# Performance work log

Hardware: AMD Instinct MI355X
Metric: run time of the kernel (lower is better)

## Reference

```python
import jax, jax.numpy as jnp
import numpy as np

EPS = 1e-05
IN_FEATURES = 1024
OUT_FEATURES = 512
M = 65536


def setup_inputs() -> dict:
    key = jax.random.key(0)
    k_x, k_w, k_b = jax.random.split(key, 3)
    x = jax.random.normal(k_x, (M, IN_FEATURES), dtype=jnp.float32)
    # kaiming_uniform(a=sqrt(5)) on [out, in]: bound = sqrt(6/((1+a^2)*fan_in)) = 1/sqrt(fan_in)
    bound = 1.0 / np.sqrt(IN_FEATURES)
    weight = jax.random.uniform(k_w, (OUT_FEATURES, IN_FEATURES), dtype=jnp.float32,
                                minval=-bound, maxval=bound)
    bias = jax.random.uniform(k_b, (OUT_FEATURES,), dtype=jnp.float32,
                              minval=-bound, maxval=bound)
    gamma = jnp.ones((OUT_FEATURES,), dtype=jnp.float32)
    beta = jnp.zeros((OUT_FEATURES,), dtype=jnp.float32)
    scale = jnp.ones((1,), dtype=jnp.float32)
    return {"x": x, "weight": weight, "bias": bias,
            "gamma": gamma, "beta": beta, "scale": scale}


def reference(x, weight, bias, gamma, beta, scale):
    # GEMM + bias: [M, N]
    acc = jnp.einsum('mk,nk->mn', x, weight) + bias[None, :]
    # Row-wise normalization over N (as the fused kernel computes per row)
    mean = jnp.mean(acc, axis=1, keepdims=True)
    var = jnp.mean((acc - mean) ** 2, axis=1, keepdims=True)
    normalized = (acc - mean) / jnp.sqrt(var + EPS)
    scaled = (normalized * gamma[None, :] + beta[None, :]) * scale[0]
    # Row softmax over N
    return jax.nn.softmax(scaled, axis=1)
```

## Files before the change

kernel.cpp:

```cpp
#include <hip/hip_runtime.h>
#include <hip/hip_bf16.h>

constexpr int KD = 1024;
constexpr int ND = 512;
constexpr int NT = 32;
constexpr float EPSV = 1e-5f;

using f32x4  = __attribute__((ext_vector_type(4))) float;
using bf16x8 = __attribute__((ext_vector_type(8))) short;
using u16x8  = __attribute__((ext_vector_type(8))) unsigned short;

__device__ __forceinline__ unsigned short f2bf(float f) {
  unsigned int u = __builtin_bit_cast(unsigned int, f);
  return (unsigned short)((u + 0x7fffu + ((u >> 16) & 1u)) >> 16);
}

__device__ __forceinline__ u16x8 pack8(float4 a, float4 b) {
  u16x8 v;
  v[0] = f2bf(a.x); v[1] = f2bf(a.y); v[2] = f2bf(a.z); v[3] = f2bf(a.w);
  v[4] = f2bf(b.x); v[5] = f2bf(b.y); v[6] = f2bf(b.z); v[7] = f2bf(b.w);
  return v;
}

__device__ __forceinline__ unsigned short cvt1(float f) {
  __hip_bfloat16 h = __float2bfloat16(f);
  return __builtin_bit_cast(unsigned short, h);
}

#define SCHEDB()  __builtin_amdgcn_sched_barrier(0)

#define BARRIER() do { \
    asm volatile("s_waitcnt lgkmcnt(0)" ::: "memory"); \
    __builtin_amdgcn_sched_barrier(0); \
    __builtin_amdgcn_s_barrier(); \
    __builtin_amdgcn_sched_barrier(0); } while (0)

__global__ void wconvert_kernel(const float* __restrict__ w,
                                unsigned short* __restrict__ wb) {
  int uid = blockIdx.x * blockDim.x + threadIdx.x;
  int s   = uid >> 11;
  int nf  = (uid >> 6) & 31;
  int l   = uid & 63;
  int n   = nf * 16 + (l & 15);
  int k0  = s * 32 + (l >> 4) * 8;
  const float* src = w + n * KD + k0;
  float4 a = *reinterpret_cast<const float4*>(src);
  float4 b = *reinterpret_cast<const float4*>(src + 4);
  *reinterpret_cast<u16x8*>(wb + (size_t)uid * 8) = pack8(a, b);
}

__global__ __launch_bounds__(512, 4)
void fused_kernel(const float* __restrict__ x,
                  const unsigned short* __restrict__ wb,
                  const float* __restrict__ bias,
                  const float* __restrict__ gamma,
                  const float* __restrict__ beta,
                  const float* __restrict__ scalep,
                  float* __restrict__ out) {
  __shared__ unsigned short As[8][64 * 32];

  const int tid  = threadIdx.x;
  const int lane = tid & 63;
  const int wid  = tid >> 6;
  const int l15  = lane & 15;
  const int lg   = lane >> 4;

  const long bm  = (long)blockIdx.x * 64;

  f32x4 acc[4][4] = {};

  const int arow = tid >> 3;
  const int akq  = tid & 7;
  const float* asrc = x + (bm + arow) * KD + akq * 4;
  const int awb = arow * 64 + (((akq >> 1) ^ ((arow >> 1) & 3)) * 16)
                + ((akq & 1) * 8);

  const int swa = (lg ^ ((l15 >> 1) & 3)) * 16;
  int ard[4];
  #pragma unroll
  for (int mi = 0; mi < 4; ++mi) ard[mi] = (mi * 16 + l15) * 64 + swa;

  const unsigned short* bbase = wb + ((size_t)(wid * 4) * 64 + lane) * 8;

#define LOADA(t) (*reinterpret_cast<const float4*>(asrc + (t) * 32))

#define LOADB(t, r0, r1, r2, r3) do { \
    const unsigned short* bp_ = bbase + (size_t)(t) * 16384; \
    r0 = *reinterpret_cast<const bf16x8*>(bp_ + 0 * 512); \
    r1 = *reinterpret_cast<const bf16x8*>(bp_ + 1 * 512); \
    r2 = *reinterpret_cast<const bf16x8*>(bp_ + 2 * 512); \
    r3 = *reinterpret_cast<const bf16x8*>(bp_ + 3 * 512); } while (0)

#define WRITE_A(q_, bufi) do { \
    union { unsigned short s[4]; unsigned long long v; } c_; \
    c_.s[0] = cvt1(q_.x); c_.s[1] = cvt1(q_.y); \
    c_.s[2] = cvt1(q_.z); c_.s[3] = cvt1(q_.w); \
    *reinterpret_cast<unsigned long long*>((char*)As[bufi] + awb) = c_.v; } while (0)

#define COMPUTE(bufi, B0, B1, B2, B3) do { \
    const char* ab_ = (const char*)As[bufi]; \
    bf16x8 a0_ = *reinterpret_cast<const bf16x8*>(ab_ + ard[0]); \
    bf16x8 a1_ = *reinterpret_cast<const bf16x8*>(ab_ + ard[1]); \
    bf16x8 a2_ = *reinterpret_cast<const bf16x8*>(ab_ + ard[2]); \
    bf16x8 a3_ = *reinterpret_cast<const bf16x8*>(ab_ + ard[3]); \
    acc[0][0] = __builtin_amdgcn_mfma_f32_16x16x32_bf16(a0_, B0, acc[0][0], 0, 0, 0); \
    acc[0][1] = __builtin_amdgcn_mfma_f32_16x16x32_bf16(a0_, B1, acc[0][1], 0, 0, 0); \
    acc[0][2] = __builtin_amdgcn_mfma_f32_16x16x32_bf16(a0_, B2, acc[0][2], 0, 0, 0); \
    acc[0][3] = __builtin_amdgcn_mfma_f32_16x16x32_bf16(a0_, B3, acc[0][3], 0, 0, 0); \
    acc[1][0] = __builtin_amdgcn_mfma_f32_16x16x32_bf16(a1_, B0, acc[1][0], 0, 0, 0); \
    acc[1][1] = __builtin_amdgcn_mfma_f32_16x16x32_bf16(a1_, B1, acc[1][1], 0, 0, 0); \
    acc[1][2] = __builtin_amdgcn_mfma_f32_16x16x32_bf16(a1_, B2, acc[1][2], 0, 0, 0); \
    acc[1][3] = __builtin_amdgcn_mfma_f32_16x16x32_bf16(a1_, B3, acc[1][3], 0, 0, 0); \
    acc[2][0] = __builtin_amdgcn_mfma_f32_16x16x32_bf16(a2_, B0, acc[2][0], 0, 0, 0); \
    acc[2][1] = __builtin_amdgcn_mfma_f32_16x16x32_bf16(a2_, B1, acc[2][1], 0, 0, 0); \
    acc[2][2] = __builtin_amdgcn_mfma_f32_16x16x32_bf16(a2_, B2, acc[2][2], 0, 0, 0); \
    acc[2][3] = __builtin_amdgcn_mfma_f32_16x16x32_bf16(a2_, B3, acc[2][3], 0, 0, 0); \
    acc[3][0] = __builtin_amdgcn_mfma_f32_16x16x32_bf16(a3_, B0, acc[3][0], 0, 0, 0); \
    acc[3][1] = __builtin_amdgcn_mfma_f32_16x16x32_bf16(a3_, B1, acc[3][1], 0, 0, 0); \
    acc[3][2] = __builtin_amdgcn_mfma_f32_16x16x32_bf16(a3_, B2, acc[3][2], 0, 0, 0); \
    acc[3][3] = __builtin_amdgcn_mfma_f32_16x16x32_bf16(a3_, B3, acc[3][3], 0, 0, 0); \
    } while (0)

  float4 qaE, qaO;
  bf16x8 bc0, bc1, bc2, bc3, bn0, bn1, bn2, bn3;

  qaE = LOADA(0);
  qaO = LOADA(1);
  WRITE_A(qaE, 0);
  WRITE_A(qaO, 1);
  qaE = LOADA(2);
  qaO = LOADA(3);
  WRITE_A(qaE, 2);
  WRITE_A(qaO, 3);
  qaE = LOADA(4);
  qaO = LOADA(5);
  LOADB(0, bc0, bc1, bc2, bc3);
  BARRIER();

  for (int t = 0; t < NT; t += 2) {
    const int tp6 = (t + 6 < NT) ? t + 6 : NT - 1;
    const int tp7 = (t + 7 < NT) ? t + 7 : NT - 1;
    WRITE_A(qaE, (t + 4) & 7);
    WRITE_A(qaO, (t + 5) & 7);
    qaE = LOADA(tp6);
    qaO = LOADA(tp7);
    LOADB(t + 1, bn0, bn1, bn2, bn3);
    SCHEDB();
    COMPUTE(t & 7, bc0, bc1, bc2, bc3);
    LOADB((t + 2 < NT) ? t + 2 : NT - 1, bc0, bc1, bc2, bc3);
    SCHEDB();
    COMPUTE((t + 1) & 7, bn0, bn1, bn2, bn3);
    BARRIER();
  }

  float* redS = (float*)As[0];
  float* redQ = redS + 576;
  float* rowA = redS + 1152;
  float* rowB = redS + 1216;

  const int col0 = wid * 64 + l15;
  const float sc = scalep[0];
  float bs4[4], gs4[4], bb4[4];
  #pragma unroll
  for (int ni = 0; ni < 4; ++ni) {
    bs4[ni] = bias[col0 + ni * 16];
    gs4[ni] = gamma[col0 + ni * 16] * sc;
    bb4[ni] = beta[col0 + ni * 16] * sc;
  }

  #pragma unroll
  for (int mi = 0; mi < 4; ++mi) {
    #pragma unroll
    for (int j = 0; j < 4; ++j) {
      float s = 0.f, q = 0.f;
      #pragma unroll
      for (int ni = 0; ni < 4; ++ni) {
        float v = acc[mi][ni][j] + bs4[ni];
        acc[mi][ni][j] = v;
        s += v;
        q = fmaf(v, v, q);
      }
      #pragma unroll
      for (int m = 1; m < 16; m <<= 1) {
        s += __shfl_xor(s, m, 64);
        q += __shfl_xor(q, m, 64);
      }
      if (l15 == 0) {
        int r = mi * 16 + lg * 4 + j;
        redS[r * 9 + wid] = s;
        redQ[r * 9 + wid] = q;
      }
    }
  }
  BARRIER();
  if (tid < 64) {
    float s = 0.f, q = 0.f;
    #pragma unroll
    for (int k = 0; k < 8; ++k) { s += redS[tid * 9 + k]; q += redQ[tid * 9 + k]; }
    float mu = s * (1.f / ND);
    rowA[tid] = mu;
    rowB[tid] = rsqrtf(q * (1.f / ND) - mu * mu + EPSV);
  }
  BARRIER();

  #pragma unroll
  for (int mi = 0; mi < 4; ++mi) {
    #pragma unroll
    for (int j = 0; j < 4; ++j) {
      int r = mi * 16 + lg * 4 + j;
      float mu = rowA[r], rs = rowB[r];
      float ps = 0.f;
      #pragma unroll
      for (int ni = 0; ni < 4; ++ni) {
        float v = (acc[mi][ni][j] - mu) * rs;
        v = fmaf(v, gs4[ni], bb4[ni]);
        float e = __expf(v);
        acc[mi][ni][j] = e;
        ps += e;
      }
      #pragma unroll
      for (int m = 1; m < 16; m <<= 1) ps += __shfl_xor(ps, m, 64);
      if (l15 == 0) redQ[r * 9 + wid] = ps;
    }
  }
  BARRIER();
  if (tid < 64) {
    float s = 0.f;
    #pragma unroll
    for (int k = 0; k < 8; ++k) s += redQ[tid * 9 + k];
    rowB[tid] = 1.f / s;
  }
  BARRIER();

  #pragma unroll
  for (int mi = 0; mi < 4; ++mi) {
    #pragma unroll
    for (int j = 0; j < 4; ++j) {
      int r = mi * 16 + lg * 4 + j;
      float rd = rowB[r];
      float* op = out + (bm + r) * ND + col0;
      #pragma unroll
      for (int ni = 0; ni < 4; ++ni)
        __builtin_nontemporal_store(acc[mi][ni][j] * rd, op + ni * 16);
    }
  }
#undef LOADA
#undef LOADB
#undef WRITE_A
#undef COMPUTE
}

__global__ void fused_fallback(const float* __restrict__ x,
                               const float* __restrict__ wf,
                               const float* __restrict__ bias,
                               const float* __restrict__ gamma,
                               const float* __restrict__ beta,
                               const float* __restrict__ scalep,
                               float* __restrict__ out) {
  long row = blockIdx.x;
  int t = threadIdx.x;
  float s = 0.f;
  const float* xr = x + row * KD;
  const float* wr_ = wf + (size_t)t * KD;
  for (int k = 0; k < KD; ++k) s += xr[k] * wr_[k];
  s += bias[t];
  __shared__ float buf[ND];
  buf[t] = s;
  __syncthreads();
  __shared__ float red[2];
  if (t == 0) {
    float sum = 0.f, sq = 0.f;
    for (int i = 0; i < ND; ++i) { sum += buf[i]; sq += buf[i] * buf[i]; }
    float mu = sum / ND;
    red[0] = mu;
    red[1] = rsqrtf(sq / ND - mu * mu + EPSV);
  }
  __syncthreads();
  float zv = (s - red[0]) * red[1] * gamma[t] * scalep[0] + beta[t] * scalep[0];
  buf[t] = zv;
  __syncthreads();
  __shared__ float red2[2];
  if (t == 0) {
    float mxv = -3.4e38f;
    for (int i = 0; i < ND; ++i) mxv = fmaxf(mxv, buf[i]);
    float den = 0.f;
    for (int i = 0; i < ND; ++i) den += __expf(buf[i] - mxv);
    red2[0] = mxv; red2[1] = 1.f / den;
  }
  __syncthreads();
  out[row * ND + t] = __expf(zv - red2[0]) * red2[1];
}

extern "C" void kernel_launch(void* const* d_in, const int* in_sizes, int n_in,
                              void* d_out, int out_size, void* d_ws, size_t ws_size,
                              hipStream_t stream) {
  const float* x     = (const float*)d_in[0];
  const float* w     = (const float*)d_in[1];
  const float* bias  = (const float*)d_in[2];
  const float* gamma = (const float*)d_in[3];
  const float* beta  = (const float*)d_in[4];
  const float* scale = (const float*)d_in[5];
  float* out = (float*)d_out;

  const int Mrows = in_sizes[0] / KD;
  const size_t wb_bytes = (size_t)ND * KD * sizeof(unsigned short);

  if (ws_size >= wb_bytes) {
    unsigned short* wbuf = (unsigned short*)d_ws;
    wconvert_kernel<<<(ND * KD / 8) / 256, 256, 0, stream>>>(w, wbuf);
    fused_kernel<<<Mrows / 64, 512, 0, stream>>>(x, wbuf, bias, gamma, beta,
                                                 scale, out);
  } else {
    fused_fallback<<<Mrows, ND, 0, stream>>>(x, w, bias, gamma, beta, scale, out);
  }
}
```

Before: 116.1 us.

## Shrink row tile to 32 with 4 waves each covering 128 columns

The fused GEMM+layernorm+softmax kernel now processes 32 rows per block with 256 threads, and each wave covers 128 output columns (2x8 MFMA tiles) instead of 64 (4x4). B fragments are reloaded in two halves interleaved with the MFMA halves, so the next tile's weights are prefetched while the current half computes. The aim is more blocks and less LDS per block, with each A fragment reused across more B tiles. In exchange, every block streams the full weight matrix for only 32 rows, which doubles total weight traffic per row.

```diff
diff --git a/kernel.cpp b/kernel.cpp
--- a/kernel.cpp
+++ b/kernel.cpp
@@ -49,7 +49,7 @@
   *reinterpret_cast<u16x8*>(wb + (size_t)uid * 8) = pack8(a, b);
 }
 
-__global__ __launch_bounds__(512, 4)
+__global__ __launch_bounds__(256, 4)
 void fused_kernel(const float* __restrict__ x,
                   const unsigned short* __restrict__ wb,
                   const float* __restrict__ bias,
@@ -57,7 +57,7 @@
                   const float* __restrict__ beta,
                   const float* __restrict__ scalep,
                   float* __restrict__ out) {
-  __shared__ unsigned short As[8][64 * 32];
+  __shared__ unsigned short As[8][32 * 32];
 
   const int tid  = threadIdx.x;
   const int lane = tid & 63;
@@ -65,9 +65,9 @@
   const int l15  = lane & 15;
   const int lg   = lane >> 4;
 
-  const long bm  = (long)blockIdx.x * 64;
-
-  f32x4 acc[4][4] = {};
+  const long bm  = (long)blockIdx.x * 32;
+
+  f32x4 acc[2][8] = {};
 
   const int arow = tid >> 3;
   const int akq  = tid & 7;
@@ -76,16 +76,15 @@
                 + ((akq & 1) * 8);
 
   const int swa = (lg ^ ((l15 >> 1) & 3)) * 16;
-  int ard[4];
-  #pragma unroll
-  for (int mi = 0; mi < 4; ++mi) ard[mi] = (mi * 16 + l15) * 64 + swa;
-
-  const unsigned short* bbase = wb + ((size_t)(wid * 4) * 64 + lane) * 8;
+  const int ard0 = (0 * 16 + l15) * 64 + swa;
+  const int ard1 = (1 * 16 + l15) * 64 + swa;
+
+  const unsigned short* bbase = wb + ((size_t)(wid * 8) * 64 + lane) * 8;
 
 #define LOADA(t) (*reinterpret_cast<const float4*>(asrc + (t) * 32))
 
-#define LOADB(t, r0, r1, r2, r3) do { \
-    const unsigned short* bp_ = bbase + (size_t)(t) * 16384; \
+#define LOADB4(t, o, r0, r1, r2, r3) do { \
+    const unsigned short* bp_ = bbase + (size_t)(t) * 16384 + (o) * 512; \
     r0 = *reinterpret_cast<const bf16x8*>(bp_ + 0 * 512); \
     r1 = *reinterpret_cast<const bf16x8*>(bp_ + 1 * 512); \
     r2 = *reinterpret_cast<const bf16x8*>(bp_ + 2 * 512); \
@@ -97,32 +96,29 @@
     c_.s[2] = cvt1(q_.z); c_.s[3] = cvt1(q_.w); \
     *reinterpret_cast<unsigned long long*>((char*)As[bufi] + awb) = c_.v; } while (0)
 
-#define COMPUTE(bufi, B0, B1, B2, B3) do { \
+#define HALF(o, b0, b1, b2, b3) do { \
+    acc[0][(o)+0] = __builtin_amdgcn_mfma_f32_16x16x32_bf16(a0_, b0, acc[0][(o)+0], 0, 0, 0); \
+    acc[0][(o)+1] = __builtin_amdgcn_mfma_f32_16x16x32_bf16(a0_, b1, acc[0][(o)+1], 0, 0, 0); \
+    acc[0][(o)+2] = __builtin_amdgcn_mfma_f32_16x16x32_bf16(a0_, b2, acc[0][(o)+2], 0, 0, 0); \
+    acc[0][(o)+3] = __builtin_amdgcn_mfma_f32_16x16x32_bf16(a0_, b3, acc[0][(o)+3], 0, 0, 0); \
+    acc[1][(o)+0] = __builtin_amdgcn_mfma_f32_16x16x32_bf16(a1_, b0, acc[1][(o)+0], 0, 0, 0); \
+    acc[1][(o)+1] = __builtin_amdgcn_mfma_f32_16x16x32_bf16(a1_, b1, acc[1][(o)+1], 0, 0, 0); \
+    acc[1][(o)+2] = __builtin_amdgcn_mfma_f32_16x16x32_bf16(a1_, b2, acc[1][(o)+2], 0, 0, 0); \
+    acc[1][(o)+3] = __builtin_amdgcn_mfma_f32_16x16x32_bf16(a1_, b3, acc[1][(o)+3], 0, 0, 0); \
+    } while (0)
+
+#define TILE(bufi, tnext) do { \
     const char* ab_ = (const char*)As[bufi]; \
-    bf16x8 a0_ = *reinterpret_cast<const bf16x8*>(ab_ + ard[0]); \
-    bf16x8 a1_ = *reinterpret_cast<const bf16x8*>(ab_ + ard[1]); \
-    bf16x8 a2_ = *reinterpret_cast<const bf16x8*>(ab_ + ard[2]); \
-    bf16x8 a3_ = *reinterpret_cast<const bf16x8*>(ab_ + ard[3]); \
-    acc[0][0] = __builtin_amdgcn_mfma_f32_16x16x32_bf16(a0_, B0, acc[0][0], 0, 0, 0); \
-    acc[0][1] = __builtin_amdgcn_mfma_f32_16x16x32_bf16(a0_, B1, acc[0][1], 0, 0, 0); \
-    acc[0][2] = __builtin_amdgcn_mfma_f32_16x16x32_bf16(a0_, B2, acc[0][2], 0, 0, 0); \
-    acc[0][3] = __builtin_amdgcn_mfma_f32_16x16x32_bf16(a0_, B3, acc[0][3], 0, 0, 0); \
-    acc[1][0] = __builtin_amdgcn_mfma_f32_16x16x32_bf16(a1_, B0, acc[1][0], 0, 0, 0); \
-    acc[1][1] = __builtin_amdgcn_mfma_f32_16x16x32_bf16(a1_, B1, acc[1][1], 0, 0, 0); \
-    acc[1][2] = __builtin_amdgcn_mfma_f32_16x16x32_bf16(a1_, B2, acc[1][2], 0, 0, 0); \
-    acc[1][3] = __builtin_amdgcn_mfma_f32_16x16x32_bf16(a1_, B3, acc[1][3], 0, 0, 0); \
-    acc[2][0] = __builtin_amdgcn_mfma_f32_16x16x32_bf16(a2_, B0, acc[2][0], 0, 0, 0); \
-    acc[2][1] = __builtin_amdgcn_mfma_f32_16x16x32_bf16(a2_, B1, acc[2][1], 0, 0, 0); \
-    acc[2][2] = __builtin_amdgcn_mfma_f32_16x16x32_bf16(a2_, B2, acc[2][2], 0, 0, 0); \
-    acc[2][3] = __builtin_amdgcn_mfma_f32_16x16x32_bf16(a2_, B3, acc[2][3], 0, 0, 0); \
-    acc[3][0] = __builtin_amdgcn_mfma_f32_16x16x32_bf16(a3_, B0, acc[3][0], 0, 0, 0); \
-    acc[3][1] = __builtin_amdgcn_mfma_f32_16x16x32_bf16(a3_, B1, acc[3][1], 0, 0, 0); \
-    acc[3][2] = __builtin_amdgcn_mfma_f32_16x16x32_bf16(a3_, B2, acc[3][2], 0, 0, 0); \
-    acc[3][3] = __builtin_amdgcn_mfma_f32_16x16x32_bf16(a3_, B3, acc[3][3], 0, 0, 0); \
+    bf16x8 a0_ = *reinterpret_cast<const bf16x8*>(ab_ + ard0); \
+    bf16x8 a1_ = *reinterpret_cast<const bf16x8*>(ab_ + ard1); \
+    HALF(0, pA0, pA1, pA2, pA3); \
+    LOADB4(tnext, 0, pA0, pA1, pA2, pA3); \
+    HALF(4, pB0, pB1, pB2, pB3); \
+    LOADB4(tnext, 4, pB0, pB1, pB2, pB3); \
     } while (0)
 
   float4 qaE, qaO;
-  bf16x8 bc0, bc1, bc2, bc3, bn0, bn1, bn2, bn3;
+  bf16x8 pA0, pA1, pA2, pA3, pB0, pB1, pB2, pB3;
 
   qaE = LOADA(0);
   qaO = LOADA(1);
@@ -134,7 +130,8 @@
   WRITE_A(qaO, 3);
   qaE = LOADA(4);
   qaO = LOADA(5);
-  LOADB(0, bc0, bc1, bc2, bc3);
+  LOADB4(0, 0, pA0, pA1, pA2, pA3);
+  LOADB4(0, 4, pB0, pB1, pB2, pB3);
   BARRIER();
 
   for (int t = 0; t < NT; t += 2) {
@@ -144,38 +141,35 @@
     WRITE_A(qaO, (t + 5) & 7);
     qaE = LOADA(tp6);
     qaO = LOADA(tp7);
-    LOADB(t + 1, bn0, bn1, bn2, bn3);
     SCHEDB();
-    COMPUTE(t & 7, bc0, bc1, bc2, bc3);
-    LOADB((t + 2 < NT) ? t + 2 : NT - 1, bc0, bc1, bc2, bc3);
-    SCHEDB();
-    COMPUTE((t + 1) & 7, bn0, bn1, bn2, bn3);
+    TILE(t & 7, t + 1);
+    TILE((t + 1) & 7, (t + 2 < NT) ? t + 2 : NT - 1);
     BARRIER();
   }
 
   float* redS = (float*)As[0];
-  float* redQ = redS + 576;
-  float* rowA = redS + 1152;
-  float* rowB = redS + 1216;
-
-  const int col0 = wid * 64 + l15;
+  float* redQ = redS + 160;
+  float* rowA = redS + 320;
+  float* rowB = redS + 352;
+
+  const int col0 = wid * 128 + l15;
   const float sc = scalep[0];
-  float bs4[4], gs4[4], bb4[4];
+  float bs8[8], gs8[8], bb8[8];
   #pragma unroll
-  for (int ni = 0; ni < 4; ++ni) {
-    bs4[ni] = bias[col0 + ni * 16];
-    gs4[ni] = gamma[col0 + ni * 16] * sc;
-    bb4[ni] = beta[col0 + ni * 16] * sc;
+  for (int ni = 0; ni < 8; ++ni) {
+    bs8[ni] = bias[col0 + ni * 16];
+    gs8[ni] = gamma[col0 + ni * 16] * sc;
+    bb8[ni] = beta[col0 + ni * 16] * sc;
   }
 
   #pragma unroll
-  for (int mi = 0; mi < 4; ++mi) {
+  for (int mi = 0; mi < 2; ++mi) {
     #pragma unroll
     for (int j = 0; j < 4; ++j) {
       float s = 0.f, q = 0.f;
       #pragma unroll
-      for (int ni = 0; ni < 4; ++ni) {
-        float v = acc[mi][ni][j] + bs4[ni];
+      for (int ni = 0; ni < 8; ++ni) {
+        float v = acc[mi][ni][j] + bs8[ni];
         acc[mi][ni][j] = v;
         s += v;
         q = fmaf(v, v, q);
@@ -187,16 +181,16 @@
       }
       if (l15 == 0) {
         int r = mi * 16 + lg * 4 + j;
-        redS[r * 9 + wid] = s;
-        redQ[r * 9 + wid] = q;
+        redS[r * 5 + wid] = s;
+        redQ[r * 5 + wid] = q;
       }
     }
   }
   BARRIER();
-  if (tid < 64) {
+  if (tid < 32) {
     float s = 0.f, q = 0.f;
     #pragma unroll
-    for (int k = 0; k < 8; ++k) { s += redS[tid * 9 + k]; q += redQ[tid * 9 + k]; }
+    for (int k = 0; k < 4; ++k) { s += redS[tid * 5 + k]; q += redQ[tid * 5 + k]; }
     float mu = s * (1.f / ND);
     rowA[tid] = mu;
     rowB[tid] = rsqrtf(q * (1.f / ND) - mu * mu + EPSV);
@@ -204,50 +198,51 @@
   BARRIER();
 
   #pragma unroll
-  for (int mi = 0; mi < 4; ++mi) {
+  for (int mi = 0; mi < 2; ++mi) {
     #pragma unroll
     for (int j = 0; j < 4; ++j) {
       int r = mi * 16 + lg * 4 + j;
       float mu = rowA[r], rs = rowB[r];
       float ps = 0.f;
       #pragma unroll
-      for (int ni = 0; ni < 4; ++ni) {
+      for (int ni = 0; ni < 8; ++ni) {
         float v = (acc[mi][ni][j] - mu) * rs;
-        v = fmaf(v, gs4[ni], bb4[ni]);
+        v = fmaf(v, gs8[ni], bb8[ni]);
         float e = __expf(v);
         acc[mi][ni][j] = e;
         ps += e;
       }
       #pragma unroll
       for (int m = 1; m < 16; m <<= 1) ps += __shfl_xor(ps, m, 64);
-      if (l15 == 0) redQ[r * 9 + wid] = ps;
+      if (l15 == 0) redQ[r * 5 + wid] = ps;
     }
   }
   BARRIER();
-  if (tid < 64) {
+  if (tid < 32) {
     float s = 0.f;
     #pragma unroll
-    for (int k = 0; k < 8; ++k) s += redQ[tid * 9 + k];
+    for (int k = 0; k < 4; ++k) s += redQ[tid * 5 + k];
     rowB[tid] = 1.f / s;
   }
   BARRIER();
 
   #pragma unroll
-  for (int mi = 0; mi < 4; ++mi) {
+  for (int mi = 0; mi < 2; ++mi) {
     #pragma unroll
     for (int j = 0; j < 4; ++j) {
       int r = mi * 16 + lg * 4 + j;
       float rd = rowB[r];
       float* op = out + (bm + r) * ND + col0;
       #pragma unroll
-      for (int ni = 0; ni < 4; ++ni)
+      for (int ni = 0; ni < 8; ++ni)
         __builtin_nontemporal_store(acc[mi][ni][j] * rd, op + ni * 16);
     }
   }
 #undef LOADA
-#undef LOADB
+#undef LOADB4
 #undef WRITE_A
-#undef COMPUTE
+#undef HALF
+#undef TILE
 }
 
 __global__ void fused_fallback(const float* __restrict__ x,
@@ -308,7 +303,7 @@
   if (ws_size >= wb_bytes) {
     unsigned short* wbuf = (unsigned short*)d_ws;
     wconvert_kernel<<<(ND * KD / 8) / 256, 256, 0, stream>>>(w, wbuf);
-    fused_kernel<<<Mrows / 64, 512, 0, stream>>>(x, wbuf, bias, gamma, beta,
+    fused_kernel<<<Mrows / 32, 256, 0, stream>>>(x, wbuf, bias, gamma, beta,
                                                  scale, out);
   } else {
     fused_fallback<<<Mrows, ND, 0, stream>>>(x, w, bias, gamma, beta, scale, out);
```

New measurement: 134.4 us. +15.8%, slower.

## Stage half of A tile into LDS at once, drop per-iteration barriers

Applied to the files above, without the earlier changes.

The 8-deep rolling LDS ring for the A operand, which needed a barrier every two k-steps, is replaced by two phases. Each phase loads half of K (16 k-steps) of A into a 16-slot LDS buffer, then runs the MFMA loop with no barriers. Only B register prefetch overlaps with compute, and LDS use doubles to 64 KB per block. That may cut occupancy and exposes the A load latency at each phase boundary.

```diff
diff --git a/kernel.cpp b/kernel.cpp
--- a/kernel.cpp
+++ b/kernel.cpp
@@ -57,7 +57,7 @@
                   const float* __restrict__ beta,
                   const float* __restrict__ scalep,
                   float* __restrict__ out) {
-  __shared__ unsigned short As[8][64 * 32];
+  __shared__ unsigned short As[16][64 * 32];
 
   const int tid  = threadIdx.x;
   const int lane = tid & 63;
@@ -81,8 +81,6 @@
   for (int mi = 0; mi < 4; ++mi) ard[mi] = (mi * 16 + l15) * 64 + swa;
 
   const unsigned short* bbase = wb + ((size_t)(wid * 4) * 64 + lane) * 8;
-
-#define LOADA(t) (*reinterpret_cast<const float4*>(asrc + (t) * 32))
 
 #define LOADB(t, r0, r1, r2, r3) do { \
     const unsigned short* bp_ = bbase + (size_t)(t) * 16384; \
@@ -96,6 +94,16 @@
     c_.s[0] = cvt1(q_.x); c_.s[1] = cvt1(q_.y); \
     c_.s[2] = cvt1(q_.z); c_.s[3] = cvt1(q_.w); \
     *reinterpret_cast<unsigned long long*>((char*)As[bufi] + awb) = c_.v; } while (0)
+
+#define STAGE_G(h, g) do { \
+    qa0 = *reinterpret_cast<const float4*>(asrc + (h) * 512 + ((g) * 4 + 0) * 32); \
+    qa1 = *reinterpret_cast<const float4*>(asrc + (h) * 512 + ((g) * 4 + 1) * 32); \
+    qa2 = *reinterpret_cast<const float4*>(asrc + (h) * 512 + ((g) * 4 + 2) * 32); \
+    qa3 = *reinterpret_cast<const float4*>(asrc + (h) * 512 + ((g) * 4 + 3) * 32); \
+    WRITE_A(qa0, (g) * 4 + 0); \
+    WRITE_A(qa1, (g) * 4 + 1); \
+    WRITE_A(qa2, (g) * 4 + 2); \
+    WRITE_A(qa3, (g) * 4 + 3); } while (0)
 
 #define COMPUTE(bufi, B0, B1, B2, B3) do { \
     const char* ab_ = (const char*)As[bufi]; \
@@ -121,37 +129,41 @@
     acc[3][3] = __builtin_amdgcn_mfma_f32_16x16x32_bf16(a3_, B3, acc[3][3], 0, 0, 0); \
     } while (0)
 
-  float4 qaE, qaO;
+  float4 qa0, qa1, qa2, qa3;
   bf16x8 bc0, bc1, bc2, bc3, bn0, bn1, bn2, bn3;
 
-  qaE = LOADA(0);
-  qaO = LOADA(1);
-  WRITE_A(qaE, 0);
-  WRITE_A(qaO, 1);
-  qaE = LOADA(2);
-  qaO = LOADA(3);
-  WRITE_A(qaE, 2);
-  WRITE_A(qaO, 3);
-  qaE = LOADA(4);
-  qaO = LOADA(5);
+  STAGE_G(0, 0);
+  STAGE_G(0, 1);
+  STAGE_G(0, 2);
+  STAGE_G(0, 3);
   LOADB(0, bc0, bc1, bc2, bc3);
   BARRIER();
 
-  for (int t = 0; t < NT; t += 2) {
-    const int tp6 = (t + 6 < NT) ? t + 6 : NT - 1;
-    const int tp7 = (t + 7 < NT) ? t + 7 : NT - 1;
-    WRITE_A(qaE, (t + 4) & 7);
-    WRITE_A(qaO, (t + 5) & 7);
-    qaE = LOADA(tp6);
-    qaO = LOADA(tp7);
-    LOADB(t + 1, bn0, bn1, bn2, bn3);
+  for (int u = 0; u < 16; u += 2) {
+    LOADB(u + 1, bn0, bn1, bn2, bn3);
     SCHEDB();
-    COMPUTE(t & 7, bc0, bc1, bc2, bc3);
-    LOADB((t + 2 < NT) ? t + 2 : NT - 1, bc0, bc1, bc2, bc3);
+    COMPUTE(u, bc0, bc1, bc2, bc3);
+    LOADB(u + 2, bc0, bc1, bc2, bc3);
     SCHEDB();
-    COMPUTE((t + 1) & 7, bn0, bn1, bn2, bn3);
-    BARRIER();
-  }
+    COMPUTE(u + 1, bn0, bn1, bn2, bn3);
+  }
+
+  BARRIER();
+  STAGE_G(1, 0);
+  STAGE_G(1, 1);
+  STAGE_G(1, 2);
+  STAGE_G(1, 3);
+  BARRIER();
+
+  for (int u = 0; u < 16; u += 2) {
+    LOADB(17 + u, bn0, bn1, bn2, bn3);
+    SCHEDB();
+    COMPUTE(u, bc0, bc1, bc2, bc3);
+    LOADB((18 + u < NT) ? 18 + u : NT - 1, bc0, bc1, bc2, bc3);
+    SCHEDB();
+    COMPUTE(u + 1, bn0, bn1, bn2, bn3);
+  }
+  BARRIER();
 
   float* redS = (float*)As[0];
   float* redQ = redS + 576;
@@ -244,9 +256,9 @@
         __builtin_nontemporal_store(acc[mi][ni][j] * rd, op + ni * 16);
     }
   }
-#undef LOADA
 #undef LOADB
 #undef WRITE_A
+#undef STAGE_G
 #undef COMPUTE
 }
 
```

Result: no change. 116.2 us (+0.1%).
